# Optimization experiments

Measured on AMD Instinct MI355X. Metric: run time of the kernel, lower is better.

Reference implementation:

```python
import jax, jax.numpy as jnp
import numpy as np

B, T = 2, 1024
V, D, H, L = 32000, 1024, 16, 8
DH = D // H  # 64
ROPE_BASE = 1000.0
EPS = 1e-6


def _rms_norm(x):
    # F.rms_norm(x, (C,), eps=1e-6)
    ms = jnp.mean(jnp.square(x), axis=-1, keepdims=True)
    return x * jax.lax.rsqrt(ms + EPS)


def _rope_tables(t_len):
    quarter = DH // 4
    inv_freq = jnp.concatenate([
        ROPE_BASE ** (-jnp.arange(quarter, dtype=jnp.float32) / quarter),
        jnp.zeros(quarter, dtype=jnp.float32),
    ])  # [DH/2]
    theta = jnp.arange(t_len, dtype=jnp.float32)[:, None] * inv_freq[None, :]  # [T, DH/2]
    return jnp.cos(theta), jnp.sin(theta)


def _apply_rope(x, cos, sin):
    # x: [B, H, T, DH]; cos/sin: [T, DH/2] broadcast to [1,1,T,DH/2]
    half = DH // 2
    x1, x2 = x[..., :half], x[..., half:]
    c = cos[None, None]
    s = sin[None, None]
    return jnp.concatenate([c * x1 - s * x2, s * x1 + c * x2], axis=-1).astype(x.dtype)


def setup_inputs() -> dict:
    key = jax.random.key(0)
    ks = jax.random.split(key, 7)
    s = 0.02
    return {
        "x_indices": jax.random.randint(ks[0], (B, T), 0, V, dtype=jnp.int32),
        "embedding": jax.random.normal(ks[1], (V, D), dtype=jnp.float32) * s,
        "Wqkv": jax.random.normal(ks[2], (L, 3 * D, D), dtype=jnp.float32) * s,
        "Wout": jax.random.normal(ks[3], (L, D, D), dtype=jnp.float32) * s,
        "W1": jax.random.normal(ks[4], (L, 4 * D, D), dtype=jnp.float32) * s,
        "W2": jax.random.normal(ks[5], (L, D, 4 * D), dtype=jnp.float32) * s,
        "lm_head": jax.random.normal(ks[6], (V, D), dtype=jnp.float32) * s,
    }


def reference(x_indices, embedding, Wqkv, Wout, W1, W2, lm_head):
    x = embedding[x_indices]  # [B, T, D]
    cos, sin = _rope_tables(T)
    causal = jnp.tril(jnp.ones((T, T), dtype=bool))  # [T, T]
    neg = jnp.finfo(x.dtype).min
    scale = 1.0 / np.sqrt(DH)

    for l in range(L):
        n = _rms_norm(x)
        qkv = jnp.einsum('btd,ed->bte', n, Wqkv[l])  # [B, T, 3D]
        qkv = qkv.reshape(B, T, 3, H, DH)
        q = jnp.transpose(qkv[:, :, 0], (0, 2, 1, 3))  # [B, H, T, DH]
        k = jnp.transpose(qkv[:, :, 1], (0, 2, 1, 3))
        v = jnp.transpose(qkv[:, :, 2], (0, 2, 1, 3))
        q = _apply_rope(q, cos, sin)
        k = _apply_rope(k, cos, sin)
        scores = jnp.einsum('bhqd,bhkd->bhqk', q, k) * scale
        scores = jnp.where(causal[None, None], scores, neg)
        attn = jax.nn.softmax(scores, axis=-1)
        ctx = jnp.einsum('bhqk,bhkd->bhqd', attn, v)
        ctx = jnp.transpose(ctx, (0, 2, 1, 3)).reshape(B, T, D)
        x = x + jnp.einsum('btd,ed->bte', ctx, Wout[l])
        n = _rms_norm(x)
        h = jnp.square(jax.nn.relu(jnp.einsum('btd,fd->btf', n, W1[l])))  # [B, T, 4D]
        x = x + jnp.einsum('btf,df->btd', h, W2[l])

    logits = jnp.einsum('btd,vd->btv', _rms_norm(x), lm_head)
    return logits.astype(jnp.float32)
```

## Files before the change

kernel.cpp:

```cpp
#include <hip/hip_runtime.h>
#include <hip/hip_bf16.h>
#include <cmath>
#include <cstdint>

#define B_  2
#define T_  1024
#define V_  32000
#define D_  1024
#define H_  16
#define L_  8
#define DH_ 64

typedef __attribute__((ext_vector_type(8))) short bf16x8;
typedef __attribute__((ext_vector_type(4))) float f32x4;

__device__ __forceinline__ ushort f2bf(float f) {
    union { float f; uint32_t u; } v; v.f = f;
    uint32_t r = v.u + 0x7FFFu + ((v.u >> 16) & 1u);
    return (ushort)(r >> 16);
}
__device__ __forceinline__ float bf2f(ushort u) {
    union { uint32_t u; float f; } v; v.u = ((uint32_t)u) << 16;
    return v.f;
}

__device__ __forceinline__ void async_copy16(const void* g, void* l) {
    __builtin_amdgcn_global_load_lds(
        (const __attribute__((address_space(1))) void*)g,
        (__attribute__((address_space(3))) void*)l, 16, 0, 0);
}

__global__ __launch_bounds__(256) void k_cast(const float4* __restrict__ in,
                                              ushort4* __restrict__ out, int n4) {
    for (int i = blockIdx.x * 256 + threadIdx.x; i < n4; i += gridDim.x * 256) {
        float4 v = in[i];
        out[i] = make_ushort4(f2bf(v.x), f2bf(v.y), f2bf(v.z), f2bf(v.w));
    }
}

__global__ void k_rope_tables(float* __restrict__ cosT, float* __restrict__ sinT) {
    int t = blockIdx.x;
    int i = threadIdx.x;
    float invf = (i < 16) ? powf(1000.0f, -(float)i / 16.0f) : 0.0f;
    float th = (float)t * invf;
    cosT[t * 32 + i] = cosf(th);
    sinT[t * 32 + i] = sinf(th);
}

__global__ __launch_bounds__(256) void k_gather(const int* __restrict__ idx,
                                                const float* __restrict__ emb,
                                                float* __restrict__ x) {
    int row = blockIdx.x;
    int id = idx[row];
    const float4* src = (const float4*)(emb + (size_t)id * D_);
    float4* dst = (float4*)(x + (size_t)row * D_);
    dst[threadIdx.x] = src[threadIdx.x];
}

__global__ __launch_bounds__(256) void k_rmsnorm(const float* __restrict__ x,
                                                 ushort* __restrict__ out) {
    int row = blockIdx.x;
    const float4* xr = (const float4*)(x + (size_t)row * D_);
    float4 v = xr[threadIdx.x];
    float ss = v.x * v.x + v.y * v.y + v.z * v.z + v.w * v.w;
    #pragma unroll
    for (int off = 1; off < 64; off <<= 1) ss += __shfl_xor(ss, off);
    __shared__ float wsum[4];
    int lane = threadIdx.x & 63, wv = threadIdx.x >> 6;
    if (lane == 0) wsum[wv] = ss;
    __syncthreads();
    float tot = wsum[0] + wsum[1] + wsum[2] + wsum[3];
    float inv = rsqrtf(tot * (1.0f / D_) + 1e-6f);
    ushort4 r = make_ushort4(f2bf(v.x * inv), f2bf(v.y * inv), f2bf(v.z * inv), f2bf(v.w * inv));
    *(ushort4*)(out + (size_t)row * D_ + threadIdx.x * 4) = r;
}

template<int BN, int EPI, bool OUTBF, bool CONVB>
__global__ __launch_bounds__(256, 2) void k_mfma_gemm(const ushort* __restrict__ A,
                                                      const void* __restrict__ Wp,
                                                      void* __restrict__ Cp,
                                                      const float* __restrict__ Res,
                                                      const float* __restrict__ cosT,
                                                      const float* __restrict__ sinT,
                                                      int M, int N, int K) {
    constexpr int BM = 128;
    constexpr int MI = 4;
    constexpr int NI = BN / 32;
    constexpr bool DBUF = (BN <= 128);
    constexpr int NB = DBUF ? 2 : 1;
    __shared__ ushort As[NB][BM][64];
    __shared__ ushort Bs[NB][BN][64];
    const int tid = threadIdx.x;
    const int wid = tid >> 6, lane = tid & 63;
    const int wr = wid >> 1, wc = wid & 1;
    const int r16 = lane & 15, kc = lane >> 4;
    const int rx = (r16 & 7) << 4;
    const int srow8 = tid >> 3;
    const int sdcp = tid & 7;

    const int nwg = gridDim.x * gridDim.y;
    int orig = blockIdx.y * gridDim.x + blockIdx.x;
    int swz = (nwg & 7) ? orig : ((orig & 7) * (nwg >> 3) + (orig >> 3));
    const size_t bm = (size_t)(swz % gridDim.x) * BM;
    const size_t bn = (size_t)(swz / gridDim.x) * BN;

    auto stage = [&](int buf, int k0) {
        #pragma unroll
        for (int i = 0; i < 4; i++) {
            const int row = i * 32 + srow8;
            const ushort* g = A + (bm + row) * (size_t)K + k0 + ((sdcp ^ (row & 7)) * 8);
            async_copy16(g, (char*)As + buf * (BM * 128) + (i * 256 + tid) * 16);
        }
        if constexpr (!CONVB) {
            const ushort* Wb = (const ushort*)Wp;
            #pragma unroll
            for (int i = 0; i < BN / 32; i++) {
                const int row = i * 32 + srow8;
                const ushort* g = Wb + (bn + row) * (size_t)K + k0 + ((sdcp ^ (row & 7)) * 8);
                async_copy16(g, (char*)Bs + buf * (BN * 128) + (i * 256 + tid) * 16);
            }
        } else {
            const float* Wf = (const float*)Wp;
            #pragma unroll
            for (int i = 0; i < BN / 32; i++) {
                const int row = i * 32 + srow8;
                const float* src = Wf + (bn + row) * (size_t)K + k0 + sdcp * 8;
                float4 v0 = *(const float4*)(src);
                float4 v1 = *(const float4*)(src + 4);
                union { ushort u[8]; bf16x8 v; } tmp;
                tmp.u[0] = f2bf(v0.x); tmp.u[1] = f2bf(v0.y);
                tmp.u[2] = f2bf(v0.z); tmp.u[3] = f2bf(v0.w);
                tmp.u[4] = f2bf(v1.x); tmp.u[5] = f2bf(v1.y);
                tmp.u[6] = f2bf(v1.z); tmp.u[7] = f2bf(v1.w);
                *(bf16x8*)((char*)Bs + buf * (BN * 128) + row * 128 + ((sdcp ^ (row & 7)) << 4)) = tmp.v;
            }
        }
    };

    f32x4 acc[MI][NI];
    #pragma unroll
    for (int mi = 0; mi < MI; mi++)
        #pragma unroll
        for (int ni = 0; ni < NI; ni++) {
            f32x4 z = {0.f, 0.f, 0.f, 0.f};
            acc[mi][ni] = z;
        }

    auto compute = [&](int buf) {
        #pragma unroll
        for (int kk = 0; kk < 2; kk++) {
            bf16x8 af[MI], bfr[NI];
            #pragma unroll
            for (int mi = 0; mi < MI; mi++)
                af[mi] = *(const bf16x8*)((const char*)As + buf * (BM * 128) +
                                          (wr * 64 + mi * 16 + r16) * 128 +
                                          ((kk * 64 + kc * 16) ^ rx));
            #pragma unroll
            for (int ni = 0; ni < NI; ni++)
                bfr[ni] = *(const bf16x8*)((const char*)Bs + buf * (BN * 128) +
                                           (wc * (BN / 2) + ni * 16 + r16) * 128 +
                                           ((kk * 64 + kc * 16) ^ rx));
            #pragma unroll
            for (int mi = 0; mi < MI; mi++)
                #pragma unroll
                for (int ni = 0; ni < NI; ni++)
                    acc[mi][ni] = __builtin_amdgcn_mfma_f32_16x16x32_bf16(af[mi], bfr[ni],
                                                                          acc[mi][ni], 0, 0, 0);
        }
    };

    const int KSTEPS = K >> 6;
    if constexpr (DBUF) {
        stage(0, 0);
        __syncthreads();
        for (int step = 0; step < KSTEPS; ++step) {
            const int cur = step & 1;
            if (step + 1 < KSTEPS) stage(cur ^ 1, (step + 1) << 6);
            compute(cur);
            __syncthreads();
        }
    } else {
        for (int step = 0; step < KSTEPS; ++step) {
            stage(0, step << 6);
            __syncthreads();
            compute(0);
            __syncthreads();
        }
    }

    #pragma unroll
    for (int mi = 0; mi < MI; mi++) {
        #pragma unroll
        for (int j = 0; j < 4; j++) {
            const size_t row = bm + wr * 64 + mi * 16 + (lane >> 4) * 4 + j;
            if constexpr (EPI == 3) {
                static_assert(BN == 128, "rope epilogue assumes BN=128");
                const int sec = (int)((bn + wc * 64) >> 10);
                if (sec < 2) {
                    const int t = (int)(row & (T_ - 1));
                    #pragma unroll
                    for (int np = 0; np < 2; np++) {
                        const int i1 = np * 16 + r16;
                        float c = cosT[t * 32 + i1], s = sinT[t * 32 + i1];
                        float x1 = acc[mi][np][j], x2 = acc[mi][np + 2][j];
                        acc[mi][np][j]     = c * x1 - s * x2;
                        acc[mi][np + 2][j] = s * x1 + c * x2;
                    }
                }
            }
            #pragma unroll
            for (int ni = 0; ni < NI; ni++) {
                const size_t col = bn + wc * (BN / 2) + ni * 16 + r16;
                float v = acc[mi][ni][j];
                if constexpr (EPI == 1) v += Res[row * N + col];
                if constexpr (EPI == 2) { v = fmaxf(v, 0.f); v *= v; }
                if constexpr (OUTBF) {
                    ((ushort*)Cp)[row * N + col] = f2bf(v);
                } else if constexpr (EPI == 0) {
                    __builtin_nontemporal_store(v, (float*)Cp + row * N + col);
                } else {
                    ((float*)Cp)[row * N + col] = v;
                }
            }
        }
    }
}

__global__ __launch_bounds__(256) void k_attn_pair(const ushort* __restrict__ qkv,
                                                   ushort* __restrict__ ctx) {
    __shared__ __align__(16) char lds[32768];
    const int tid = threadIdx.x;
    const int w = tid >> 6, lane = tid & 63;
    const int r16 = lane & 15, kc = lane >> 4;
    const int rx = (r16 & 7) << 4;
    const int ip = blockIdx.x;
    const int qb[2] = { ip * 64, (15 - ip) * 64 };
    const int bh = blockIdx.y, b = bh >> 4, h = bh & 15;
    const size_t tok0 = (size_t)b * T_;
    const ushort* kg = qkv + tok0 * (3 * D_) + D_ + h * DH_;
    const ushort* vg = qkv + tok0 * (3 * D_) + 2 * D_ + h * DH_;
    const float SCALE_LOG2E = 0.125f * 1.44269504089f;

    #pragma unroll
    for (int t = 0; t < 2; t++) {
        const ushort* qg = qkv + (tok0 + qb[t]) * (3 * D_) + h * DH_;
        #pragma unroll
        for (int i = 0; i < 2; i++) {
            int slot = i * 256 + tid;
            int row = slot >> 3, dcp = slot & 7;
            int d0 = (dcp ^ (row & 7)) * 8;
            async_copy16(qg + (size_t)row * (3 * D_) + d0, lds + 16384 + t * 8192 + slot * 16);
        }
    }
    __syncthreads();
    bf16x8 aq[2][2];
    #pragma unroll
    for (int t = 0; t < 2; t++)
        #pragma unroll
        for (int ks = 0; ks < 2; ks++) {
            int row = w * 16 + r16;
            aq[t][ks] = *(const bf16x8*)(lds + 16384 + t * 8192 + row * 128 +
                                         ((ks * 64 + kc * 16) ^ rx));
        }

    f32x4 o[2][4];
    float m[2][4], l[2][4];
    #pragma unroll
    for (int t = 0; t < 2; t++)
        #pragma unroll
        for (int nd = 0; nd < 4; nd++) {
            f32x4 z = {0.f, 0.f, 0.f, 0.f};
            o[t][nd] = z;
            m[t][nd] = -1e30f; l[t][nd] = 0.f;
        }

    const int nch = 16 - ip;
    for (int ch = 0; ch < nch; ch++) {
        const int kb = ch << 6;
        __syncthreads();
        #pragma unroll
        for (int i = 0; i < 2; i++) {
            int slot = i * 256 + tid;
            int row = slot >> 3, dcp = slot & 7;
            int d0 = (dcp ^ (row & 7)) * 8;
            async_copy16(kg + (size_t)(kb + row) * (3 * D_) + d0, lds + slot * 16);
        }
        {
            int key = tid >> 2, dbase = (tid & 3) * 16;
            const ushort* src = vg + (size_t)(kb + key) * (3 * D_) + dbase;
            bf16x8 v0 = *(const bf16x8*)(src);
            bf16x8 v1 = *(const bf16x8*)(src + 8);
            #pragma unroll
            for (int e = 0; e < 8; e++) {
                int d = dbase + e;
                *(ushort*)(lds + 8192 + d * 128 + ((key * 2) ^ ((d & 7) << 4))) = (ushort)v0[e];
                d = dbase + 8 + e;
                *(ushort*)(lds + 8192 + d * 128 + ((key * 2) ^ ((d & 7) << 4))) = (ushort)v1[e];
            }
        }
        __syncthreads();

        const int nact = (ch <= ip) ? 2 : 1;
        for (int tt = 0; tt < nact; tt++) {
            const int t = (tt == 0) ? 1 : 0;
            const int pq = 16384 + t * 8192;
            f32x4 s[4];
            #pragma unroll
            for (int ni = 0; ni < 4; ni++) { f32x4 z = {0.f, 0.f, 0.f, 0.f}; s[ni] = z; }
            __builtin_amdgcn_s_setprio(1);
            #pragma unroll
            for (int ks = 0; ks < 2; ks++)
                #pragma unroll
                for (int ni = 0; ni < 4; ni++) {
                    int row = ni * 16 + r16;
                    bf16x8 kf = *(const bf16x8*)(lds + row * 128 + ((ks * 64 + kc * 16) ^ rx));
                    s[ni] = __builtin_amdgcn_mfma_f32_16x16x32_bf16(aq[t][ks], kf, s[ni], 0, 0, 0);
                }
            __builtin_amdgcn_s_setprio(0);

            const bool diag = (kb == qb[t]);
            float corr[4];
            #pragma unroll
            for (int j = 0; j < 4; j++) {
                const int qrow = qb[t] + w * 16 + kc * 4 + j;
                #pragma unroll
                for (int ni = 0; ni < 4; ni++) {
                    float v = s[ni][j] * SCALE_LOG2E;
                    if (diag) { int key = kb + ni * 16 + r16; if (key > qrow) v = -1e30f; }
                    s[ni][j] = v;
                }
                float tmax = fmaxf(fmaxf(s[0][j], s[1][j]), fmaxf(s[2][j], s[3][j]));
                #pragma unroll
                for (int off = 1; off < 16; off <<= 1) tmax = fmaxf(tmax, __shfl_xor(tmax, off));
                float mn = fmaxf(m[t][j], tmax);
                corr[j] = exp2f(m[t][j] - mn);
                m[t][j] = mn;
                float ps = 0.f;
                #pragma unroll
                for (int ni = 0; ni < 4; ni++) {
                    float p = exp2f(s[ni][j] - mn);
                    s[ni][j] = p;
                    ps += p;
                }
                #pragma unroll
                for (int off = 1; off < 16; off <<= 1) ps += __shfl_xor(ps, off);
                l[t][j] = l[t][j] * corr[j] + ps;
            }
            #pragma unroll
            for (int ni = 0; ni < 4; ni++)
                #pragma unroll
                for (int j = 0; j < 4; j++) {
                    int row = w * 16 + kc * 4 + j;
                    *(ushort*)(lds + pq + row * 128 + ((ni * 32 + r16 * 2) ^ ((row & 7) << 4))) = f2bf(s[ni][j]);
                }
            #pragma unroll
            for (int nd = 0; nd < 4; nd++)
                #pragma unroll
                for (int j = 0; j < 4; j++) o[t][nd][j] *= corr[j];
            __builtin_amdgcn_s_setprio(1);
            #pragma unroll
            for (int ks = 0; ks < 2; ks++) {
                int prow = w * 16 + r16;
                bf16x8 pf = *(const bf16x8*)(lds + pq + prow * 128 + ((ks * 64 + kc * 16) ^ rx));
                #pragma unroll
                for (int nd = 0; nd < 4; nd++) {
                    int drow = nd * 16 + r16;
                    bf16x8 vf = *(const bf16x8*)(lds + 8192 + drow * 128 + ((ks * 64 + kc * 16) ^ rx));
                    o[t][nd] = __builtin_amdgcn_mfma_f32_16x16x32_bf16(pf, vf, o[t][nd], 0, 0, 0);
                }
            }
            __builtin_amdgcn_s_setprio(0);
        }
    }

    #pragma unroll
    for (int t = 0; t < 2; t++)
        #pragma unroll
        for (int j = 0; j < 4; j++) {
            float inv = 1.0f / l[t][j];
            int row = qb[t] + w * 16 + kc * 4 + j;
            ushort* dst = ctx + (tok0 + row) * D_ + h * DH_;
            #pragma unroll
            for (int nd = 0; nd < 4; nd++)
                dst[nd * 16 + r16] = f2bf(o[t][nd][j] * inv);
        }
}

extern "C" void kernel_launch(void* const* d_in, const int* in_sizes, int n_in,
                              void* d_out, int out_size, void* d_ws, size_t ws_size,
                              hipStream_t stream) {
    const int*   xi   = (const int*)d_in[0];
    const float* emb  = (const float*)d_in[1];
    const float* Wqkv = (const float*)d_in[2];
    const float* Wout = (const float*)d_in[3];
    const float* W1   = (const float*)d_in[4];
    const float* W2   = (const float*)d_in[5];
    const float* lmh  = (const float*)d_in[6];
    float* out = (float*)d_out;

    const size_t NT = (size_t)B_ * T_;
    size_t off = 0;
    auto carve = [&](size_t bytes) -> char* {
        char* r = (char*)d_ws + off;
        off += (bytes + 255) & ~(size_t)255;
        return r;
    };
    float*  xbuf = (float*)carve(NT * D_ * 4);
    ushort* qkv  = (ushort*)carve(NT * 3 * D_ * 2);
    ushort* nb   = (ushort*)carve(NT * D_ * 2);
    ushort* ctxb = (ushort*)carve(NT * D_ * 2);
    ushort* hb   = (ushort*)carve(NT * 4 * D_ * 2);
    float*  cosT = (float*)carve(T_ * 32 * 4);
    float*  sinT = (float*)carve(T_ * 32 * 4);

    const size_t nWqkv = (size_t)L_ * 3 * D_ * D_;
    const size_t nWout = (size_t)L_ * D_ * D_;
    const size_t nW1   = (size_t)L_ * 4 * D_ * D_;
    const size_t nW2   = (size_t)L_ * 4 * D_ * D_;
    const size_t nLmh  = (size_t)V_ * D_;
    ushort* WqkvB = (ushort*)carve(nWqkv * 2);
    ushort* WoutB = (ushort*)carve(nWout * 2);
    ushort* W1B   = (ushort*)carve(nW1 * 2);
    ushort* W2B   = (ushort*)carve(nW2 * 2);
    ushort* lmhB  = (ushort*)carve(nLmh * 2);
    const bool preconv = (off <= ws_size);

    if (preconv) {
        k_cast<<<dim3(2048), dim3(256), 0, stream>>>((const float4*)Wqkv, (ushort4*)WqkvB, (int)(nWqkv / 4));
        k_cast<<<dim3(2048), dim3(256), 0, stream>>>((const float4*)Wout, (ushort4*)WoutB, (int)(nWout / 4));
        k_cast<<<dim3(2048), dim3(256), 0, stream>>>((const float4*)W1,   (ushort4*)W1B,   (int)(nW1 / 4));
        k_cast<<<dim3(2048), dim3(256), 0, stream>>>((const float4*)W2,   (ushort4*)W2B,   (int)(nW2 / 4));
        k_cast<<<dim3(2048), dim3(256), 0, stream>>>((const float4*)lmh,  (ushort4*)lmhB,  (int)(nLmh / 4));
    }

#define LAUNCH_GEMM(BN, EPI, OUTBF, GX, GY, Aq, Wb16, Wf32, Cq, Rq, Mv, Nv, Kv)              \
    do {                                                                                     \
        if (preconv)                                                                         \
            k_mfma_gemm<BN, EPI, OUTBF, false><<<dim3(GX, GY), dim3(256), 0, stream>>>(      \
                (const ushort*)(Aq), (const void*)(Wb16), (void*)(Cq), (Rq), cosT, sinT,     \
                Mv, Nv, Kv);                                                                 \
        else                                                                                 \
            k_mfma_gemm<BN, EPI, OUTBF, true><<<dim3(GX, GY), dim3(256), 0, stream>>>(       \
                (const ushort*)(Aq), (const void*)(Wf32), (void*)(Cq), (Rq), cosT, sinT,     \
                Mv, Nv, Kv);                                                                 \
    } while (0)

    k_rope_tables<<<dim3(T_), dim3(32), 0, stream>>>(cosT, sinT);
    k_gather<<<dim3(NT), dim3(256), 0, stream>>>(xi, emb, xbuf);

    for (int l = 0; l < L_; l++) {
        k_rmsnorm<<<dim3(NT), dim3(256), 0, stream>>>(xbuf, nb);
        LAUNCH_GEMM(128, 3, true, 16, 24, nb,
                    WqkvB + (size_t)l * 3 * D_ * D_, Wqkv + (size_t)l * 3 * D_ * D_,
                    qkv, nullptr, (int)NT, 3 * D_, D_);
        k_attn_pair<<<dim3(8, B_ * H_), dim3(256), 0, stream>>>(qkv, ctxb);
        LAUNCH_GEMM(64, 1, false, 16, 16, ctxb,
                    WoutB + (size_t)l * D_ * D_, Wout + (size_t)l * D_ * D_,
                    xbuf, xbuf, (int)NT, D_, D_);
        k_rmsnorm<<<dim3(NT), dim3(256), 0, stream>>>(xbuf, nb);
        LAUNCH_GEMM(128, 2, true, 16, 32, nb,
                    W1B + (size_t)l * 4 * D_ * D_, W1 + (size_t)l * 4 * D_ * D_,
                    hb, nullptr, (int)NT, 4 * D_, D_);
        LAUNCH_GEMM(64, 1, false, 16, 16, hb,
                    W2B + (size_t)l * 4 * D_ * D_, W2 + (size_t)l * 4 * D_ * D_,
                    xbuf, xbuf, (int)NT, D_, 4 * D_);
    }
    k_rmsnorm<<<dim3(NT), dim3(256), 0, stream>>>(xbuf, nb);
    LAUNCH_GEMM(256, 0, false, 16, 125, nb, lmhB, lmh, out, nullptr, (int)NT, V_, D_);
#undef LAUNCH_GEMM
}
```

Before: 1.877 ms.

## Fuse RMSNorm into GEMM epilogues via row sum-of-squares and deferred scaling

Removes the standalone rmsnorm kernels. The residual-producing GEMMs (Wout, W2) and the gather now write an unnormalized bf16 copy of x and atomically accumulate per-row sums of squares. The consuming GEMMs (QKV, W1, lm_head) apply the rsqrt scale per row in the epilogue, since the norm is a per-row scalar that commutes with the matmul. This trades 17 small kernel launches and the extra x reads for atomics, extra bf16 stores in the epilogue, and slightly different rounding, because unnormalized values are quantized to bf16 before scaling.

Measured after the change: 1.943 ms. 1.03x slower.

```diff
diff --git a/kernel.cpp b/kernel.cpp
--- a/kernel.cpp
+++ b/kernel.cpp
@@ -49,39 +49,35 @@
 
 __global__ __launch_bounds__(256) void k_gather(const int* __restrict__ idx,
                                                 const float* __restrict__ emb,
-                                                float* __restrict__ x) {
+                                                float* __restrict__ x,
+                                                ushort* __restrict__ xb,
+                                                float* __restrict__ ss) {
     int row = blockIdx.x;
     int id = idx[row];
-    const float4* src = (const float4*)(emb + (size_t)id * D_);
-    float4* dst = (float4*)(x + (size_t)row * D_);
-    dst[threadIdx.x] = src[threadIdx.x];
-}
-
-__global__ __launch_bounds__(256) void k_rmsnorm(const float* __restrict__ x,
-                                                 ushort* __restrict__ out) {
-    int row = blockIdx.x;
-    const float4* xr = (const float4*)(x + (size_t)row * D_);
-    float4 v = xr[threadIdx.x];
-    float ss = v.x * v.x + v.y * v.y + v.z * v.z + v.w * v.w;
-    #pragma unroll
-    for (int off = 1; off < 64; off <<= 1) ss += __shfl_xor(ss, off);
+    float4 v = ((const float4*)(emb + (size_t)id * D_))[threadIdx.x];
+    ((float4*)(x + (size_t)row * D_))[threadIdx.x] = v;
+    *(ushort4*)(xb + (size_t)row * D_ + threadIdx.x * 4) =
+        make_ushort4(f2bf(v.x), f2bf(v.y), f2bf(v.z), f2bf(v.w));
+    float s = v.x * v.x + v.y * v.y + v.z * v.z + v.w * v.w;
+    #pragma unroll
+    for (int off = 1; off < 64; off <<= 1) s += __shfl_xor(s, off);
     __shared__ float wsum[4];
     int lane = threadIdx.x & 63, wv = threadIdx.x >> 6;
-    if (lane == 0) wsum[wv] = ss;
+    if (lane == 0) wsum[wv] = s;
     __syncthreads();
-    float tot = wsum[0] + wsum[1] + wsum[2] + wsum[3];
-    float inv = rsqrtf(tot * (1.0f / D_) + 1e-6f);
-    ushort4 r = make_ushort4(f2bf(v.x * inv), f2bf(v.y * inv), f2bf(v.z * inv), f2bf(v.w * inv));
-    *(ushort4*)(out + (size_t)row * D_ + threadIdx.x * 4) = r;
-}
-
-template<int BN, int EPI, bool OUTBF, bool CONVB>
+    if (threadIdx.x == 0) ss[row] = wsum[0] + wsum[1] + wsum[2] + wsum[3];
+}
+
+template<int BN, int EPI, bool OUTBF, bool CONVB, bool RSCALE, bool SSOUT>
 __global__ __launch_bounds__(256, 2) void k_mfma_gemm(const ushort* __restrict__ A,
                                                       const void* __restrict__ Wp,
                                                       void* __restrict__ Cp,
                                                       const float* __restrict__ Res,
                                                       const float* __restrict__ cosT,
                                                       const float* __restrict__ sinT,
+                                                      const float* __restrict__ ssIn,
+                                                      float* __restrict__ ssOut,
+                                                      ushort* __restrict__ xbOut,
                                                       int M, int N, int K) {
     constexpr int BM = 128;
     constexpr int MI = 4;
@@ -193,6 +189,11 @@
         #pragma unroll
         for (int j = 0; j < 4; j++) {
             const size_t row = bm + wr * 64 + mi * 16 + (lane >> 4) * 4 + j;
+            if constexpr (RSCALE) {
+                const float sc = rsqrtf(ssIn[row] * (1.0f / 1024.0f) + 1e-6f);
+                #pragma unroll
+                for (int ni = 0; ni < NI; ni++) acc[mi][ni][j] *= sc;
+            }
             if constexpr (EPI == 3) {
                 static_assert(BN == 128, "rope epilogue assumes BN=128");
                 const int sec = (int)((bn + wc * 64) >> 10);
@@ -208,12 +209,17 @@
                     }
                 }
             }
+            float ssq = 0.f;
             #pragma unroll
             for (int ni = 0; ni < NI; ni++) {
                 const size_t col = bn + wc * (BN / 2) + ni * 16 + r16;
                 float v = acc[mi][ni][j];
                 if constexpr (EPI == 1) v += Res[row * N + col];
                 if constexpr (EPI == 2) { v = fmaxf(v, 0.f); v *= v; }
+                if constexpr (SSOUT) {
+                    ssq += v * v;
+                    xbOut[row * N + col] = f2bf(v);
+                }
                 if constexpr (OUTBF) {
                     ((ushort*)Cp)[row * N + col] = f2bf(v);
                 } else if constexpr (EPI == 0) {
@@ -221,6 +227,11 @@
                 } else {
                     ((float*)Cp)[row * N + col] = v;
                 }
+            }
+            if constexpr (SSOUT) {
+                #pragma unroll
+                for (int off = 1; off < 16; off <<= 1) ssq += __shfl_xor(ssq, off);
+                if (r16 == 0) atomicAdd(&ssOut[row], ssq);
             }
         }
     }
@@ -406,12 +417,15 @@
         return r;
     };
     float*  xbuf = (float*)carve(NT * D_ * 4);
+    ushort* xb   = (ushort*)carve(NT * D_ * 2);
     ushort* qkv  = (ushort*)carve(NT * 3 * D_ * 2);
-    ushort* nb   = (ushort*)carve(NT * D_ * 2);
     ushort* ctxb = (ushort*)carve(NT * D_ * 2);
     ushort* hb   = (ushort*)carve(NT * 4 * D_ * 2);
     float*  cosT = (float*)carve(T_ * 32 * 4);
     float*  sinT = (float*)carve(T_ * 32 * 4);
+    float*  ssA  = (float*)carve(17 * NT * 4);
+    float*  ss_q = ssA;
+    float*  ss_f = ssA + 9 * NT;
 
     const size_t nWqkv = (size_t)L_ * 3 * D_ * D_;
     const size_t nWout = (size_t)L_ * D_ * D_;
@@ -425,6 +439,8 @@
     ushort* lmhB  = (ushort*)carve(nLmh * 2);
     const bool preconv = (off <= ws_size);
 
+    hipMemsetAsync(ssA, 0, 17 * NT * 4, stream);
+
     if (preconv) {
         k_cast<<<dim3(2048), dim3(256), 0, stream>>>((const float4*)Wqkv, (ushort4*)WqkvB, (int)(nWqkv / 4));
         k_cast<<<dim3(2048), dim3(256), 0, stream>>>((const float4*)Wout, (ushort4*)WoutB, (int)(nWout / 4));
@@ -433,39 +449,37 @@
         k_cast<<<dim3(2048), dim3(256), 0, stream>>>((const float4*)lmh,  (ushort4*)lmhB,  (int)(nLmh / 4));
     }
 
-#define LAUNCH_GEMM(BN, EPI, OUTBF, GX, GY, Aq, Wb16, Wf32, Cq, Rq, Mv, Nv, Kv)              \
+#define LAUNCH_GEMM(BN, EPI, OUTBF, RSC, SSO, GX, GY, Aq, Wb16, Wf32, Cq, Rq, ssin, ssout, xbo, Mv, Nv, Kv) \
     do {                                                                                     \
         if (preconv)                                                                         \
-            k_mfma_gemm<BN, EPI, OUTBF, false><<<dim3(GX, GY), dim3(256), 0, stream>>>(      \
+            k_mfma_gemm<BN, EPI, OUTBF, false, RSC, SSO><<<dim3(GX, GY), dim3(256), 0, stream>>>( \
                 (const ushort*)(Aq), (const void*)(Wb16), (void*)(Cq), (Rq), cosT, sinT,     \
-                Mv, Nv, Kv);                                                                 \
+                (ssin), (ssout), (xbo), Mv, Nv, Kv);                                         \
         else                                                                                 \
-            k_mfma_gemm<BN, EPI, OUTBF, true><<<dim3(GX, GY), dim3(256), 0, stream>>>(       \
+            k_mfma_gemm<BN, EPI, OUTBF, true, RSC, SSO><<<dim3(GX, GY), dim3(256), 0, stream>>>( \
                 (const ushort*)(Aq), (const void*)(Wf32), (void*)(Cq), (Rq), cosT, sinT,     \
-                Mv, Nv, Kv);                                                                 \
+                (ssin), (ssout), (xbo), Mv, Nv, Kv);                                         \
     } while (0)
 
     k_rope_tables<<<dim3(T_), dim3(32), 0, stream>>>(cosT, sinT);
-    k_gather<<<dim3(NT), dim3(256), 0, stream>>>(xi, emb, xbuf);
+    k_gather<<<dim3(NT), dim3(256), 0, stream>>>(xi, emb, xbuf, xb, ss_q);
 
     for (int l = 0; l < L_; l++) {
-        k_rmsnorm<<<dim3(NT), dim3(256), 0, stream>>>(xbuf, nb);
-        LAUNCH_GEMM(128, 3, true, 16, 24, nb,
+        LAUNCH_GEMM(128, 3, true, true, false, 16, 24, xb,
                     WqkvB + (size_t)l * 3 * D_ * D_, Wqkv + (size_t)l * 3 * D_ * D_,
-                    qkv, nullptr, (int)NT, 3 * D_, D_);
+                    qkv, nullptr, ss_q + (size_t)l * NT, nullptr, nullptr, (int)NT, 3 * D_, D_);
         k_attn_pair<<<dim3(8, B_ * H_), dim3(256), 0, stream>>>(qkv, ctxb);
-        LAUNCH_GEMM(64, 1, false, 16, 16, ctxb,
+        LAUNCH_GEMM(64, 1, false, false, true, 16, 16, ctxb,
                     WoutB + (size_t)l * D_ * D_, Wout + (size_t)l * D_ * D_,
-                    xbuf, xbuf, (int)NT, D_, D_);
-        k_rmsnorm<<<dim3(NT), dim3(256), 0, stream>>>(xbuf, nb);
-        LAUNCH_GEMM(128, 2, true, 16, 32, nb,
+                    xbuf, xbuf, nullptr, ss_f + (size_t)l * NT, xb, (int)NT, D_, D_);
+        LAUNCH_GEMM(128, 2, true, true, false, 16, 32, xb,
                     W1B + (size_t)l * 4 * D_ * D_, W1 + (size_t)l * 4 * D_ * D_,
-                    hb, nullptr, (int)NT, 4 * D_, D_);
-        LAUNCH_GEMM(64, 1, false, 16, 16, hb,
+                    hb, nullptr, ss_f + (size_t)l * NT, nullptr, nullptr, (int)NT, 4 * D_, D_);
+        LAUNCH_GEMM(64, 1, false, false, true, 16, 16, hb,
                     W2B + (size_t)l * 4 * D_ * D_, W2 + (size_t)l * 4 * D_ * D_,
-                    xbuf, xbuf, (int)NT, D_, 4 * D_);
-    }
-    k_rmsnorm<<<dim3(NT), dim3(256), 0, stream>>>(xbuf, nb);
-    LAUNCH_GEMM(256, 0, false, 16, 125, nb, lmhB, lmh, out, nullptr, (int)NT, V_, D_);
+                    xbuf, xbuf, nullptr, ss_q + (size_t)(l + 1) * NT, xb, (int)NT, D_, 4 * D_);
+    }
+    LAUNCH_GEMM(256, 0, false, true, false, 16, 125, xb, lmhB, lmh, out, nullptr,
+                ss_q + (size_t)L_ * NT, nullptr, nullptr, (int)NT, V_, D_);
 #undef LAUNCH_GEMM
 }
```

## Add 256x256-tile 8-wave GEMM kernel for the lm_head projection

Applied to the files above, without the earlier changes.

Adds a dedicated bf16 MFMA GEMM for the final vocab projection. It uses 256x256 output tiles, 512 threads, double-buffered swizzled LDS staging and an interleaved schedule of async copies and MFMAs, with grouped workgroup ordering for L2 reuse. The kernel is used only when bf16 pre-converted weights are available. The larger tile is meant to raise arithmetic intensity and overlap loads with compute, at the cost of higher register and LDS pressure and lower occupancy.

Measured after the change: 1.878 ms. About the same (+0.0%).

```diff
diff --git a/kernel.cpp b/kernel.cpp
--- a/kernel.cpp
+++ b/kernel.cpp
@@ -226,6 +226,114 @@
     }
 }
 
+__global__ __launch_bounds__(512, 2) void k_gemm256(const ushort* __restrict__ A,
+                                                    const ushort* __restrict__ Wb,
+                                                    float* __restrict__ C,
+                                                    int M, int N, int K) {
+    __shared__ ushort As[2][256][64];
+    __shared__ ushort Bs[2][256][64];
+    constexpr int BUFB = 256 * 64 * 2;
+    const int tid = threadIdx.x;
+    const int wid = tid >> 6, lane = tid & 63;
+    const int wr = wid >> 2, wc = wid & 3;
+    const int r16 = lane & 15, kc = lane >> 4;
+    const int rx = (r16 & 7) << 4;
+
+    const int nwg = gridDim.x * gridDim.y;
+    int orig = blockIdx.y * gridDim.x + blockIdx.x;
+    int swz = (nwg & 7) ? orig : ((orig & 7) * (nwg >> 3) + (orig >> 3));
+    const size_t bm = (size_t)(swz % gridDim.x) * 256;
+    const size_t bn = (size_t)(swz / gridDim.x) * 256;
+
+    auto stageq = [&](int buf, int k0, int q) {
+        const int s = q * 512 + tid;
+        const int row = s >> 3, ch = s & 7;
+        const int col = (ch ^ (row & 7)) * 8;
+        async_copy16(A + (bm + row) * (size_t)K + k0 + col, (char*)As + buf * BUFB + s * 16);
+        async_copy16(Wb + (bn + row) * (size_t)K + k0 + col, (char*)Bs + buf * BUFB + s * 16);
+    };
+
+    f32x4 acc[8][4];
+    #pragma unroll
+    for (int mi = 0; mi < 8; mi++)
+        #pragma unroll
+        for (int ni = 0; ni < 4; ni++) {
+            f32x4 z = {0.f, 0.f, 0.f, 0.f};
+            acc[mi][ni] = z;
+        }
+
+    const int KS = K >> 6;
+    #pragma unroll
+    for (int q = 0; q < 4; q++) stageq(0, 0, q);
+    __syncthreads();
+
+    for (int t = 0; t < KS; ++t) {
+        const int cur = t & 1, nxt = cur ^ 1;
+        const bool pre = (t + 1 < KS);
+        const char* Ab = (const char*)As + cur * BUFB;
+        const char* Bb = (const char*)Bs + cur * BUFB;
+
+        bf16x8 af[4][2], bf0[2][2], bf1[2][2];
+
+        auto loadA = [&](int half) {
+            #pragma unroll
+            for (int mi = 0; mi < 4; mi++)
+                #pragma unroll
+                for (int kk = 0; kk < 2; kk++)
+                    af[mi][kk] = *(const bf16x8*)(Ab + (wr * 128 + half * 64 + mi * 16 + r16) * 128 +
+                                                  ((kk * 64 + kc * 16) ^ rx));
+        };
+        auto loadB = [&](bf16x8 (&bf)[2][2], int half) {
+            #pragma unroll
+            for (int ni = 0; ni < 2; ni++)
+                #pragma unroll
+                for (int kk = 0; kk < 2; kk++)
+                    bf[ni][kk] = *(const bf16x8*)(Bb + (wc * 64 + half * 32 + ni * 16 + r16) * 128 +
+                                                  ((kk * 64 + kc * 16) ^ rx));
+        };
+        auto quad = [&](int mh, bf16x8 (&bf)[2][2], int nh) {
+            __builtin_amdgcn_s_setprio(1);
+            #pragma unroll
+            for (int kk = 0; kk < 2; kk++)
+                #pragma unroll
+                for (int mi = 0; mi < 4; mi++)
+                    #pragma unroll
+                    for (int ni = 0; ni < 2; ni++)
+                        acc[mh * 4 + mi][nh * 2 + ni] =
+                            __builtin_amdgcn_mfma_f32_16x16x32_bf16(af[mi][kk], bf[ni][kk],
+                                                                    acc[mh * 4 + mi][nh * 2 + ni], 0, 0, 0);
+            __builtin_amdgcn_s_setprio(0);
+        };
+
+        if (pre) stageq(nxt, (t + 1) << 6, 0);
+        loadA(0); loadB(bf0, 0);
+        quad(0, bf0, 0);
+        if (pre) stageq(nxt, (t + 1) << 6, 1);
+        loadB(bf1, 1);
+        quad(0, bf1, 1);
+        if (pre) stageq(nxt, (t + 1) << 6, 2);
+        loadA(1);
+        quad(1, bf1, 1);
+        if (pre) stageq(nxt, (t + 1) << 6, 3);
+        quad(1, bf0, 0);
+
+        __syncthreads();
+    }
+
+    #pragma unroll
+    for (int mi = 0; mi < 8; mi++) {
+        #pragma unroll
+        for (int j = 0; j < 4; j++) {
+            const size_t row = bm + wr * 128 + mi * 16 + (lane >> 4) * 4 + j;
+            #pragma unroll
+            for (int ni = 0; ni < 4; ni++) {
+                const size_t col = bn + wc * 64 + ni * 16 + r16;
+                __builtin_nontemporal_store(acc[mi][ni][j], C + row * (size_t)N + col);
+            }
+        }
+    }
+}
+
 __global__ __launch_bounds__(256) void k_attn_pair(const ushort* __restrict__ qkv,
                                                    ushort* __restrict__ ctx) {
     __shared__ __align__(16) char lds[32768];
@@ -466,6 +574,9 @@
                     xbuf, xbuf, (int)NT, D_, 4 * D_);
     }
     k_rmsnorm<<<dim3(NT), dim3(256), 0, stream>>>(xbuf, nb);
-    LAUNCH_GEMM(256, 0, false, 16, 125, nb, lmhB, lmh, out, nullptr, (int)NT, V_, D_);
+    if (preconv)
+        k_gemm256<<<dim3(8, 125), dim3(512), 0, stream>>>(nb, lmhB, out, (int)NT, V_, D_);
+    else
+        LAUNCH_GEMM(256, 0, false, 16, 125, nb, lmhB, lmh, out, nullptr, (int)NT, V_, D_);
 #undef LAUNCH_GEMM
 }
```
